# Performance work log

Hardware: AMD Instinct MI355X
Metric: run time of the kernel (lower is better)

Reference implementation:

```python
import jax, jax.numpy as jnp
import numpy as np

B, T, C, HR = 8, 4096, 256, 4
N_LAYER, LAYER_ID = 12, 3
HID = HR * C


def _fancy_decay_first():
    # Faithful reproduction of VRWKV_SpatialMix._init_weights(init_mode='fancy')
    r01 = LAYER_ID / (N_LAYER - 1)
    h = np.arange(C, dtype=np.float32)
    decay = -5.0 + 8.0 * (h / (C - 1)) ** (0.7 + 1.3 * r01)
    zig = ((np.arange(1, C + 1) % 3) - 1).astype(np.float32) * 0.5
    first = np.float32(np.log(0.3)) + zig
    return jnp.asarray(decay, jnp.float32), jnp.asarray(first, jnp.float32)


def setup_inputs() -> dict:
    key = jax.random.key(0)
    ks = jax.random.split(key, 12)
    s = 0.02  # small weight scale keeps exp(k) well-conditioned
    decay, first = _fancy_decay_first()
    return {
        "x": jax.random.normal(ks[0], (B, T, C), jnp.float32),
        "Wk": jax.random.normal(ks[1], (C, C), jnp.float32) * s,
        "Wv": jax.random.normal(ks[2], (C, C), jnp.float32) * s,
        "Wr": jax.random.normal(ks[3], (C, C), jnp.float32) * s,
        "Wo": jax.random.normal(ks[4], (C, C), jnp.float32) * s,
        "Wk_ffn": jax.random.normal(ks[5], (C, HID), jnp.float32) * s,
        "Wv_ffn": jax.random.normal(ks[6], (HID, C), jnp.float32) * s,
        "Wr_ffn": jax.random.normal(ks[7], (C, C), jnp.float32) * s,
        "g1": 1.0 + 0.1 * jax.random.normal(ks[8], (C,), jnp.float32),
        "b1": 0.1 * jax.random.normal(ks[9], (C,), jnp.float32),
        "g2": 1.0 + 0.1 * jax.random.normal(ks[10], (C,), jnp.float32),
        "b2": 0.1 * jax.random.normal(ks[11], (C,), jnp.float32),
        "spatial_decay": decay,
        "spatial_first": first,
    }


def _ln(x, g, b):
    m = jnp.mean(x, axis=-1, keepdims=True)
    v = jnp.var(x, axis=-1, keepdims=True)
    return (x - m) * jax.lax.rsqrt(v + 1e-5) * g + b


def _wkv(w, u, k, v):
    # Numerically-stable log-space WKV recurrence (same math as wkv_cuda):
    # y_t = (sum_{i<t} e^{w*(t-1-i)+k_i} v_i + e^{u+k_t} v_t)
    #     / (sum_{i<t} e^{w*(t-1-i)+k_i}     + e^{u+k_t})
    # w,u: [C]; k,v: [B,T,C] -> y: [B,T,C]
    Bb, Tt, Cc = k.shape
    kT = jnp.swapaxes(k, 0, 1)  # [T,B,C]
    vT = jnp.swapaxes(v, 0, 1)

    def step(carry, kv):
        p, q, o = carry           # [B,C] num / den / running max exponent
        kt, vt = kv               # [B,C]
        no = jnp.maximum(o, u + kt)
        A = jnp.exp(o - no)
        E = jnp.exp(u + kt - no)
        y = (A * p + E * vt) / (A * q + E)
        no2 = jnp.maximum(w + o, kt)
        A2 = jnp.exp(w + o - no2)
        E2 = jnp.exp(kt - no2)
        return (A2 * p + E2 * vt, A2 * q + E2, no2), y

    init = (jnp.zeros((Bb, Cc), k.dtype),
            jnp.zeros((Bb, Cc), k.dtype),
            jnp.full((Bb, Cc), -1e38, k.dtype))
    _, yT = jax.lax.scan(step, init, (kT, vT))
    return jnp.swapaxes(yT, 0, 1)


def reference(x, Wk, Wv, Wr, Wo, Wk_ffn, Wv_ffn, Wr_ffn, g1, b1, g2, b2,
              spatial_decay, spatial_first):
    Tlen = x.shape[1]
    # --- SpatialMix (shift_pixel=0 -> xk=xv=xr=h, key_norm=False) ---
    h = _ln(x, g1, b1)
    k = h @ Wk
    v = h @ Wv
    sr = jax.nn.sigmoid(h @ Wr)
    y = _wkv(spatial_decay / Tlen, spatial_first / Tlen, k, v)
    x = x + (sr * y) @ Wo
    # --- ChannelMix (square-ReLU MLP, sigmoid receptance gate) ---
    h2 = _ln(x, g2, b2)
    kk = jnp.square(jax.nn.relu(h2 @ Wk_ffn))
    x = x + jax.nn.sigmoid(h2 @ Wr_ffn) * (kk @ Wv_ffn)
    return x
```

## Files before the change

### kernel.cpp

```cpp
#include <hip/hip_runtime.h>
#include <hip/hip_bf16.h>
#include <math.h>

#define TDIM 4096
#define CDIM 256
#define BDIM 8
#define NTOK (BDIM * TDIM)
#define HIDDIM 1024
#define NCHUNK 256
#define CHLEN 16

typedef float f32x4 __attribute__((ext_vector_type(4)));
typedef __bf16 bf16x8 __attribute__((ext_vector_type(8)));
typedef __bf16 bf16x4 __attribute__((ext_vector_type(4)));

#define GLDS16(gp, lp) __builtin_amdgcn_global_load_lds( \
    (const __attribute__((address_space(1))) void*)(gp), \
    (__attribute__((address_space(3))) void*)(lp), 16, 0, 0)

#define WAITCNT_VM6  0x0F76
#define WAITCNT_VM5  0x0F75
#define WAITCNT_VM4  0x0F74
#define WAITCNT_VM2  0x0F72
#define WAITCNT_VM0  0x0F70
#define WAITCNT_VM20 0x4F74

__device__ __forceinline__ float sigm(float v) { return 1.0f / (1.0f + __expf(-v)); }

__global__ __launch_bounds__(256) void pack_weights(
    const float* __restrict__ Wk, const float* __restrict__ Wv,
    const float* __restrict__ Wr, const float* __restrict__ Wo,
    const float* __restrict__ Wkf, const float* __restrict__ Wvf,
    const float* __restrict__ Wrf,
    __bf16* __restrict__ WkvrT, __bf16* __restrict__ WoT,
    __bf16* __restrict__ Wkfr, unsigned char* __restrict__ Wvf8) {
  long long j = (long long)blockIdx.x * 256 + threadIdx.x;
  if (j < 196608) {
    int n = (int)(j >> 8), k = (int)(j & 255);
    const float* src = (n < 256) ? Wk : (n < 512 ? Wv : Wr);
    WkvrT[j] = (__bf16)src[k * 256 + (n & 255)];
    return;
  }
  j -= 196608;
  if (j < 65536) { int n = (int)(j >> 8), k = (int)(j & 255);
    WoT[j] = (__bf16)Wo[k * 256 + n]; return; }
  j -= 65536;
  if (j < 327680) { int n = (int)(j >> 8), k = (int)(j & 255);
    Wkfr[j] = (__bf16)(n < 1024 ? Wkf[(long long)k * 1024 + n]
                                : Wrf[k * 256 + (n - 1024)]);
    return; }
  j -= 327680;
  if (j < 65536) {
    const long long d = j * 4;
    const int n = (int)(d >> 10), k0 = (int)(d & 1023);
    int w = 0;
    w = __builtin_amdgcn_cvt_pk_fp8_f32(Wvf[(long long)k0 * 256 + n],
                                        Wvf[(long long)(k0 + 1) * 256 + n], w, false);
    w = __builtin_amdgcn_cvt_pk_fp8_f32(Wvf[(long long)(k0 + 2) * 256 + n],
                                        Wvf[(long long)(k0 + 3) * 256 + n], w, true);
    *(int*)&Wvf8[d] = w;
    return;
  }
}

__global__ __launch_bounds__(256) void ln_kernel(
    const float* __restrict__ x, const float* __restrict__ gamma,
    const float* __restrict__ beta, __bf16* __restrict__ h) {
  const int wave = threadIdx.x >> 6, lane = threadIdx.x & 63;
  const long long row = (long long)blockIdx.x * 4 + wave;
  const long long base = row * CDIM + lane * 4;
  const f32x4 v = *(const f32x4*)&x[base];
  float s = v[0] + v[1] + v[2] + v[3];
  float s2 = v[0]*v[0] + v[1]*v[1] + v[2]*v[2] + v[3]*v[3];
  #pragma unroll
  for (int o = 1; o < 64; o <<= 1) { s += __shfl_xor(s, o); s2 += __shfl_xor(s2, o); }
  const float mean = s * (1.0f / CDIM);
  const float var = s2 * (1.0f / CDIM) - mean * mean;
  const float rstd = rsqrtf(var + 1e-5f);
  const f32x4 g4 = *(const f32x4*)&gamma[lane * 4];
  const f32x4 b4 = *(const f32x4*)&beta[lane * 4];
  bf16x4 o;
  #pragma unroll
  for (int r = 0; r < 4; r++) o[r] = (__bf16)((v[r] - mean) * rstd * g4[r] + b4[r]);
  *(bf16x4*)&h[base] = o;
}

template <int BN, int EPI, int MT>
__global__ __launch_bounds__(256, 3) void gemm3(
    const __bf16* __restrict__ A, const __bf16* __restrict__ Bt,
    int M, int N,
    __bf16* __restrict__ outH, __bf16* __restrict__ outH2,
    unsigned char* __restrict__ outC) {
  constexpr int K = 256;
  constexpr int WNT = BN / 32;
  constexpr int NBC = BN / 64;
  __shared__ __bf16 sA[3][128 * 32];
  __shared__ __bf16 sB[3][BN * 32];

  const int tid = threadIdx.x;
  const int wave = tid >> 6, lane = tid & 63;
  const int quad = lane >> 4, mrow = lane & 15;
  const long long bm = (long long)blockIdx.x * (128 * MT);
  const long long bn = (long long)blockIdx.y * BN;
  const int wm = (wave & 1) * 64, wn = (wave >> 1) * (BN / 2);

  const int lrow = lane >> 2;
  const int lk = (lane & 3) * 8;

  auto issue = [&](int g) {
    const int buf = g % 3;
    const long long k0 = (long long)(g & 7) * 32;
    const long long ar = bm + (long long)(g >> 3) * 128;
    const int a0 = wave * 32;
    GLDS16(A + (ar + a0 + lrow) * (long long)K + k0 + lk, &sA[buf][a0 * 32]);
    GLDS16(A + (ar + a0 + 16 + lrow) * (long long)K + k0 + lk, &sA[buf][(a0 + 16) * 32]);
    #pragma unroll
    for (int bc = 0; bc < NBC; bc++) {
      const int r0 = wave * (BN / 4) + bc * 16;
      GLDS16(Bt + (bn + r0 + lrow) * (long long)K + k0 + lk, &sB[buf][r0 * 32]);
    }
  };

  f32x4 acc[4][WNT] = {};

  auto compute = [&](int g) {
    const int buf = g % 3;
    bf16x8 fa[4], fb[WNT];
    #pragma unroll
    for (int mt = 0; mt < 4; mt++)
      fa[mt] = *(const bf16x8*)&sA[buf][(wm + mt * 16 + mrow) * 32 + quad * 8];
    #pragma unroll
    for (int nt = 0; nt < WNT; nt++)
      fb[nt] = *(const bf16x8*)&sB[buf][(wn + nt * 16 + mrow) * 32 + quad * 8];
    #pragma unroll
    for (int mt = 0; mt < 4; mt++)
      #pragma unroll
      for (int nt = 0; nt < WNT; nt++)
        acc[mt][nt] = __builtin_amdgcn_mfma_f32_16x16x32_bf16(fb[nt], fa[mt], acc[mt][nt], 0, 0, 0);
  };

  auto epilogue = [&](int mti) {
    const long long rb0 = bm + (long long)mti * 128;
    #pragma unroll
    for (int mt = 0; mt < 4; mt++) {
      #pragma unroll
      for (int nt = 0; nt < WNT; nt++) {
        const long long row = rb0 + wm + mt * 16 + mrow;
        const int cloc = wn + nt * 16 + quad * 4;
        const long long colb = bn + cloc;
        const f32x4 a = acc[mt][nt];
        if (EPI == 0) {
          const int plane = blockIdx.y >> 1;
          __bf16* o = outH + (long long)plane * ((long long)M * 256);
          const long long c2 = colb & 255;
          bf16x4 v;
          if (plane == 2) {
            #pragma unroll
            for (int r = 0; r < 4; r++) v[r] = (__bf16)sigm(a[r]);
          } else {
            #pragma unroll
            for (int r = 0; r < 4; r++) v[r] = (__bf16)a[r];
          }
          *(bf16x4*)&o[row * 256 + c2] = v;
        } else if (EPI == 2) {
          if (blockIdx.y < 8) {
            float t0 = a[0] > 0.0f ? a[0] : 0.0f;
            float t1 = a[1] > 0.0f ? a[1] : 0.0f;
            float t2 = a[2] > 0.0f ? a[2] : 0.0f;
            float t3 = a[3] > 0.0f ? a[3] : 0.0f;
            int w = 0;
            w = __builtin_amdgcn_cvt_pk_fp8_f32(t0 * t0, t1 * t1, w, false);
            w = __builtin_amdgcn_cvt_pk_fp8_f32(t2 * t2, t3 * t3, w, true);
            *(int*)&outC[row * 1024 + colb] = w;
          } else {
            bf16x4 v;
            #pragma unroll
            for (int r = 0; r < 4; r++) v[r] = (__bf16)sigm(a[r]);
            *(bf16x4*)&outH2[row * 256 + (colb - 1024)] = v;
          }
        }
        acc[mt][nt] = (f32x4){0.0f, 0.0f, 0.0f, 0.0f};
      }
    }
  };

  constexpr int total = 8 * MT;
  issue(0);
  issue(1);

  #pragma unroll 1
  for (int g = 0; g < total; g++) {
    if (g == total - 1) {
      __builtin_amdgcn_s_waitcnt(WAITCNT_VM0);
    } else if (MT > 1 && g >= 8 && (g & 7) <= 1) {
      __builtin_amdgcn_s_waitcnt(WAITCNT_VM20);
    } else if (BN == 256) {
      __builtin_amdgcn_s_waitcnt(WAITCNT_VM6);
    } else {
      __builtin_amdgcn_s_waitcnt(WAITCNT_VM4);
    }
    __builtin_amdgcn_s_barrier();
    if (g + 2 < total) issue(g + 2);
    compute(g);
    if ((g & 7) == 7) epilogue(g >> 3);
  }
}

__global__ __launch_bounds__(256, 2) void gemm7(
    const __bf16* __restrict__ A, const __bf16* __restrict__ Bt,
    const float* __restrict__ x,
    const float* __restrict__ gammaP, const float* __restrict__ betaP,
    __bf16* __restrict__ x1h, __bf16* __restrict__ h2) {
  constexpr int K = 256;
  __shared__ __bf16 sA[3][64 * 32];
  __shared__ __bf16 sB[3][256 * 32];
  __shared__ float redS[4][64], redQ[4][64];

  const int tid = threadIdx.x;
  const int wave = tid >> 6, lane = tid & 63;
  const int quad = lane >> 4, mrow = lane & 15;
  const long long bm = (long long)blockIdx.x * 64;
  const int wn = wave * 64;
  const int lrow = lane >> 2;
  const int lk = (lane & 3) * 8;

  auto issue = [&](int g) {
    const int buf = g % 3;
    const long long k0 = (long long)g * 32;
    GLDS16(A + (bm + wave * 16 + lrow) * (long long)K + k0 + lk,
           &sA[buf][(wave * 16) * 32]);
    #pragma unroll
    for (int bc = 0; bc < 4; bc++) {
      const int r0 = wave * 64 + bc * 16;
      GLDS16(Bt + (r0 + lrow) * (long long)K + k0 + lk, &sB[buf][r0 * 32]);
    }
  };

  f32x4 acc[4][4] = {};

  auto compute = [&](int g) {
    const int buf = g % 3;
    bf16x8 fa[4], fb[4];
    #pragma unroll
    for (int mt = 0; mt < 4; mt++)
      fa[mt] = *(const bf16x8*)&sA[buf][(mt * 16 + mrow) * 32 + quad * 8];
    #pragma unroll
    for (int nt = 0; nt < 4; nt++)
      fb[nt] = *(const bf16x8*)&sB[buf][(wn + nt * 16 + mrow) * 32 + quad * 8];
    #pragma unroll
    for (int mt = 0; mt < 4; mt++)
      #pragma unroll
      for (int nt = 0; nt < 4; nt++)
        acc[mt][nt] = __builtin_amdgcn_mfma_f32_16x16x32_bf16(fb[nt], fa[mt], acc[mt][nt], 0, 0, 0);
  };

  issue(0);
  issue(1);
  #pragma unroll 1
  for (int g = 0; g < 8; g++) {
    if (g == 7) {
      __builtin_amdgcn_s_waitcnt(WAITCNT_VM0);
    } else {
      __builtin_amdgcn_s_waitcnt(WAITCNT_VM5);
    }
    __builtin_amdgcn_s_barrier();
    if (g + 2 < 8) issue(g + 2);
    compute(g);
  }

  float sum[4] = {0, 0, 0, 0}, sq[4] = {0, 0, 0, 0};
  #pragma unroll
  for (int mt = 0; mt < 4; mt++) {
    #pragma unroll
    for (int nt = 0; nt < 4; nt++) {
      const long long row = bm + mt * 16 + mrow;
      const long long colb = wn + nt * 16 + quad * 4;
      acc[mt][nt] += *(const f32x4*)&x[row * 256 + colb];
      #pragma unroll
      for (int r = 0; r < 4; r++) {
        sum[mt] += acc[mt][nt][r];
        sq[mt] += acc[mt][nt][r] * acc[mt][nt][r];
      }
    }
  }
  #pragma unroll
  for (int mt = 0; mt < 4; mt++) {
    sum[mt] += __shfl_xor(sum[mt], 16); sq[mt] += __shfl_xor(sq[mt], 16);
    sum[mt] += __shfl_xor(sum[mt], 32); sq[mt] += __shfl_xor(sq[mt], 32);
  }
  if (quad == 0) {
    #pragma unroll
    for (int mt = 0; mt < 4; mt++) {
      redS[wave][mt * 16 + mrow] = sum[mt];
      redQ[wave][mt * 16 + mrow] = sq[mt];
    }
  }
  __syncthreads();
  #pragma unroll
  for (int mt = 0; mt < 4; mt++) {
    const int rb = mt * 16 + mrow;
    const float ts = redS[0][rb] + redS[1][rb] + redS[2][rb] + redS[3][rb];
    const float tq = redQ[0][rb] + redQ[1][rb] + redQ[2][rb] + redQ[3][rb];
    const float mean = ts * (1.0f / 256.0f);
    const float rstd = rsqrtf(tq * (1.0f / 256.0f) - mean * mean + 1e-5f);
    const long long row = bm + rb;
    #pragma unroll
    for (int nt = 0; nt < 4; nt++) {
      const long long colb = wn + nt * 16 + quad * 4;
      const f32x4 g4 = *(const f32x4*)&gammaP[colb];
      const f32x4 b4 = *(const f32x4*)&betaP[colb];
      bf16x4 xo, ho;
      #pragma unroll
      for (int r = 0; r < 4; r++) {
        const float t = acc[mt][nt][r];
        xo[r] = (__bf16)t;
        ho[r] = (__bf16)((t - mean) * rstd * g4[r] + b4[r]);
      }
      *(bf16x4*)&x1h[row * 256 + colb] = xo;
      *(bf16x4*)&h2[row * 256 + colb] = ho;
    }
  }
}

__global__ __launch_bounds__(256, 4) void gemm6(
    const unsigned char* __restrict__ A8, const unsigned char* __restrict__ B8,
    float* __restrict__ outF, const __bf16* __restrict__ srcH,
    const __bf16* __restrict__ gate) {
  __shared__ unsigned char sA[3][128 * 32];
  __shared__ unsigned char sB[3][128 * 32];
  const int tid = threadIdx.x;
  const int wave = tid >> 6, lane = tid & 63;
  const int quad = lane >> 4, mrow = lane & 15;
  const long long bm = (long long)blockIdx.x * 128;
  const long long bn = (long long)blockIdx.y * 128;
  const int wm = (wave & 1) * 64, wn = (wave >> 1) * 64;
  const int srow = lane >> 1;
  const int hs = (lane & 1) ^ ((lane >> 2) & 1);

  auto issue = [&](int g) {
    const int buf = g % 3;
    const long long k0 = (long long)g * 32;
    const int a0 = wave * 32;
    GLDS16(A8 + (bm + a0 + srow) * 1024LL + k0 + hs * 16, &sA[buf][a0 * 32]);
    GLDS16(B8 + (bn + a0 + srow) * 1024LL + k0 + hs * 16, &sB[buf][a0 * 32]);
  };

  f32x4 acc[4][4] = {};
  issue(0);
  issue(1);
  const int sw = (mrow >> 1) & 1;

  auto compute = [&](int i) {
    const int buf = i % 3;
    long long fa[4], fb[4];
    const int off = ((((quad >> 1) ^ sw) << 4) | ((quad & 1) << 3));
    #pragma unroll
    for (int mt = 0; mt < 4; mt++)
      fa[mt] = *(const long long*)&sA[buf][(wm + mt * 16 + mrow) * 32 + off];
    #pragma unroll
    for (int nt = 0; nt < 4; nt++)
      fb[nt] = *(const long long*)&sB[buf][(wn + nt * 16 + mrow) * 32 + off];
    #pragma unroll
    for (int mt = 0; mt < 4; mt++)
      #pragma unroll
      for (int nt = 0; nt < 4; nt++)
        acc[mt][nt] = __builtin_amdgcn_mfma_f32_16x16x32_fp8_fp8(fb[nt], fa[mt], acc[mt][nt], 0, 0, 0);
  };

  #pragma unroll 1
  for (int i = 0; i < 31; i++) {
    __builtin_amdgcn_s_waitcnt(WAITCNT_VM2);
    __builtin_amdgcn_s_barrier();
    if (i + 2 < 32) issue(i + 2);
    compute(i);
  }
  __builtin_amdgcn_s_waitcnt(WAITCNT_VM0);
  __builtin_amdgcn_s_barrier();
  compute(31);

  #pragma unroll
  for (int mt = 0; mt < 4; mt++) {
    #pragma unroll
    for (int nt = 0; nt < 4; nt++) {
      const long long row = bm + wm + mt * 16 + mrow;
      const long long colb = bn + wn + nt * 16 + quad * 4;
      const long long idx = row * 256 + colb;
      const f32x4 a = acc[mt][nt];
      const bf16x4 s4 = *(const bf16x4*)&srcH[idx];
      const bf16x4 g4 = *(const bf16x4*)&gate[idx];
      f32x4 v;
      #pragma unroll
      for (int r = 0; r < 4; r++) v[r] = (float)s4[r] + (float)g4[r] * a[r];
      *(f32x4*)&outF[idx] = v;
    }
  }
}

__global__ __launch_bounds__(256) void wkv_phase1(
    const __bf16* __restrict__ ka, const __bf16* __restrict__ va,
    const float* __restrict__ decay,
    float* __restrict__ Sloc, float* __restrict__ Zloc) {
  const int wave = threadIdx.x >> 6, lane = threadIdx.x & 63;
  const int gi = blockIdx.x * 4 + wave;
  const int b = gi >> 8, chunk = gi & (NCHUNK - 1);
  const int c0 = lane * 4;
  const f32x4 w4 = *(const f32x4*)&decay[c0];
  f32x4 ew;
  #pragma unroll
  for (int r = 0; r < 4; r++) ew[r] = __expf(w4[r] * (1.0f / TDIM));
  f32x4 S = {0,0,0,0}, Z = {0,0,0,0};
  long long base = ((long long)b * TDIM + (long long)chunk * CHLEN) * 256 + c0;
  #pragma unroll 4
  for (int t = 0; t < CHLEN; t++) {
    const bf16x4 k4 = *(const bf16x4*)&ka[base + (long long)t * 256];
    const bf16x4 v4 = *(const bf16x4*)&va[base + (long long)t * 256];
    #pragma unroll
    for (int r = 0; r < 4; r++) {
      const float ek = __expf((float)k4[r]);
      S[r] = ew[r] * S[r] + ek * (float)v4[r];
      Z[r] = ew[r] * Z[r] + ek;
    }
  }
  const long long o = (long long)gi * 256 + c0;
  *(f32x4*)&Sloc[o] = S;
  *(f32x4*)&Zloc[o] = Z;
}

__global__ __launch_bounds__(256) void wkv_phase2(
    const float* __restrict__ Sloc, const float* __restrict__ Zloc,
    const float* __restrict__ decay,
    float* __restrict__ Sstart, float* __restrict__ Zstart) {
  const int idx = blockIdx.x * 256 + threadIdx.x;
  const int c = idx & 255;
  const int b = idx >> 8;
  const float w = decay[c] * (1.0f / TDIM);
  const float ewL = __expf(w * (float)CHLEN);
  float S = 0.0f, Z = 0.0f;
  for (int j = 0; j < NCHUNK; j++) {
    const long long o = ((long long)b * NCHUNK + j) * 256 + c;
    Sstart[o] = S;
    Zstart[o] = Z;
    S = ewL * S + Sloc[o];
    Z = ewL * Z + Zloc[o];
  }
}

__global__ __launch_bounds__(256) void wkv_phase3(
    const __bf16* __restrict__ ka, const __bf16* __restrict__ va,
    const __bf16* __restrict__ ra,
    const float* __restrict__ decay, const float* __restrict__ first,
    const float* __restrict__ Sstart, const float* __restrict__ Zstart,
    __bf16* __restrict__ a2) {
  const int wave = threadIdx.x >> 6, lane = threadIdx.x & 63;
  const int gi = blockIdx.x * 4 + wave;
  const int b = gi >> 8, chunk = gi & (NCHUNK - 1);
  const int c0 = lane * 4;
  const f32x4 w4 = *(const f32x4*)&decay[c0];
  const f32x4 u4 = *(const f32x4*)&first[c0];
  f32x4 ew, eu;
  #pragma unroll
  for (int r = 0; r < 4; r++) {
    ew[r] = __expf(w4[r] * (1.0f / TDIM));
    eu[r] = __expf(u4[r] * (1.0f / TDIM));
  }
  const long long so = (long long)gi * 256 + c0;
  f32x4 S = *(const f32x4*)&Sstart[so];
  f32x4 Z = *(const f32x4*)&Zstart[so];
  long long base = ((long long)b * TDIM + (long long)chunk * CHLEN) * 256 + c0;
  #pragma unroll 2
  for (int t = 0; t < CHLEN; t++) {
    const long long p = base + (long long)t * 256;
    const bf16x4 k4 = *(const bf16x4*)&ka[p];
    const bf16x4 v4 = *(const bf16x4*)&va[p];
    const bf16x4 r4 = *(const bf16x4*)&ra[p];
    bf16x4 o;
    #pragma unroll
    for (int r = 0; r < 4; r++) {
      const float ek = __expf((float)k4[r]);
      const float E = eu[r] * ek;
      const float y = (S[r] + E * (float)v4[r]) / (Z[r] + E);
      o[r] = (__bf16)((float)r4[r] * y);
      S[r] = ew[r] * S[r] + ek * (float)v4[r];
      Z[r] = ew[r] * Z[r] + ek;
    }
    *(bf16x4*)&a2[p] = o;
  }
}

extern "C" void kernel_launch(void* const* d_in, const int* in_sizes, int n_in,
                              void* d_out, int out_size, void* d_ws, size_t ws_size,
                              hipStream_t stream) {
  const float* x     = (const float*)d_in[0];
  const float* Wk    = (const float*)d_in[1];
  const float* Wv    = (const float*)d_in[2];
  const float* Wr    = (const float*)d_in[3];
  const float* Wo    = (const float*)d_in[4];
  const float* Wkf   = (const float*)d_in[5];
  const float* Wvf   = (const float*)d_in[6];
  const float* Wrf   = (const float*)d_in[7];
  const float* g1    = (const float*)d_in[8];
  const float* b1    = (const float*)d_in[9];
  const float* g2    = (const float*)d_in[10];
  const float* b2    = (const float*)d_in[11];
  const float* decay = (const float*)d_in[12];
  const float* first = (const float*)d_in[13];
  float* out = (float*)d_out;
  char* ws = (char*)d_ws;

  __bf16* ka     = (__bf16*)(ws + 0);
  __bf16* va     = (__bf16*)(ws + 16777216LL);
  __bf16* ra     = (__bf16*)(ws + 33554432LL);
  __bf16* a2     = (__bf16*)(ws + 50331648LL);
  __bf16* g2buf  = (__bf16*)(ws + 50331648LL);
  __bf16* hbuf   = (__bf16*)(ws + 67108864LL);
  __bf16* h2     = (__bf16*)(ws + 67108864LL);
  __bf16* x1h    = (__bf16*)(ws + 83886080LL);
  unsigned char* kk8 = (unsigned char*)(ws + 100663296LL);
  float*  Sloc   = (float*)(ws + 134217728LL);
  float*  Zloc   = (float*)(ws + 137363456LL);
  float*  Sstart = (float*)(ws + 140509184LL);
  float*  Zstart = (float*)(ws + 143654912LL);
  __bf16* WkvrT  = (__bf16*)(ws + 167772160LL);
  __bf16* WoT    = (__bf16*)(ws + 168165376LL);
  __bf16* Wkfr   = (__bf16*)(ws + 168296448LL);
  unsigned char* Wvf8 = (unsigned char*)(ws + 168951808LL);

  pack_weights<<<2560, 256, 0, stream>>>(Wk, Wv, Wr, Wo, Wkf, Wvf, Wrf,
                                         WkvrT, WoT, Wkfr, Wvf8);

  ln_kernel<<<NTOK / 4, 256, 0, stream>>>(x, g1, b1, hbuf);
  gemm3<128, 0, 2><<<dim3(NTOK / 256, 6), 256, 0, stream>>>(
      hbuf, WkvrT, NTOK, 768, ka, nullptr, nullptr);
  wkv_phase1<<<BDIM * NCHUNK / 4, 256, 0, stream>>>(ka, va, decay, Sloc, Zloc);
  wkv_phase2<<<BDIM, 256, 0, stream>>>(Sloc, Zloc, decay, Sstart, Zstart);
  wkv_phase3<<<BDIM * NCHUNK / 4, 256, 0, stream>>>(ka, va, ra, decay, first,
                                                    Sstart, Zstart, a2);
  gemm7<<<NTOK / 64, 256, 0, stream>>>(a2, WoT, x, g2, b2, x1h, h2);

  gemm3<128, 2, 2><<<dim3(NTOK / 256, 10), 256, 0, stream>>>(
      h2, Wkfr, NTOK, 1280, nullptr, g2buf, kk8);
  gemm6<<<dim3(NTOK / 128, 2), 256, 0, stream>>>(
      kk8, Wvf8, out, x1h, g2buf);
}
```

Before: 279.1 us.

## Switch LN outputs and K/V/R and FFN-in GEMMs to FP8 MFMA

Both layer-norm outputs (LN1 and the LN2 fused into gemm7) are now written as FP8, and the K/V/R and FFN key/receptance weights are packed to FP8. The bf16 gemm3 kernel is replaced by an FP8 gemm8 with 128x128 tiles and swizzled LDS reads, modeled on the existing gemm6. This halves activation and weight traffic and uses the higher-rate FP8 MFMA, at the cost of lower precision on the k, v and r projections that feed the exponential WKV recurrence.

Result: faster. 270.3 us (-3.1%).

```diff
diff --git a/kernel.cpp b/kernel.cpp
--- a/kernel.cpp
+++ b/kernel.cpp
@@ -18,12 +18,9 @@
     (const __attribute__((address_space(1))) void*)(gp), \
     (__attribute__((address_space(3))) void*)(lp), 16, 0, 0)
 
-#define WAITCNT_VM6  0x0F76
 #define WAITCNT_VM5  0x0F75
-#define WAITCNT_VM4  0x0F74
 #define WAITCNT_VM2  0x0F72
 #define WAITCNT_VM0  0x0F70
-#define WAITCNT_VM20 0x4F74
 
 __device__ __forceinline__ float sigm(float v) { return 1.0f / (1.0f + __expf(-v)); }
 
@@ -32,24 +29,45 @@
     const float* __restrict__ Wr, const float* __restrict__ Wo,
     const float* __restrict__ Wkf, const float* __restrict__ Wvf,
     const float* __restrict__ Wrf,
-    __bf16* __restrict__ WkvrT, __bf16* __restrict__ WoT,
-    __bf16* __restrict__ Wkfr, unsigned char* __restrict__ Wvf8) {
+    __bf16* __restrict__ WoT, unsigned char* __restrict__ Wkvr8,
+    unsigned char* __restrict__ Wkfr8, unsigned char* __restrict__ Wvf8) {
   long long j = (long long)blockIdx.x * 256 + threadIdx.x;
-  if (j < 196608) {
-    int n = (int)(j >> 8), k = (int)(j & 255);
+  if (j < 49152) {
+    const long long d = j * 4;
+    const int n = (int)(d >> 8), k0 = (int)(d & 255);
     const float* src = (n < 256) ? Wk : (n < 512 ? Wv : Wr);
-    WkvrT[j] = (__bf16)src[k * 256 + (n & 255)];
+    const int nn = n & 255;
+    int w = 0;
+    w = __builtin_amdgcn_cvt_pk_fp8_f32(src[k0 * 256 + nn],
+                                        src[(k0 + 1) * 256 + nn], w, false);
+    w = __builtin_amdgcn_cvt_pk_fp8_f32(src[(k0 + 2) * 256 + nn],
+                                        src[(k0 + 3) * 256 + nn], w, true);
+    *(int*)&Wkvr8[d] = w;
     return;
   }
-  j -= 196608;
+  j -= 49152;
   if (j < 65536) { int n = (int)(j >> 8), k = (int)(j & 255);
     WoT[j] = (__bf16)Wo[k * 256 + n]; return; }
   j -= 65536;
-  if (j < 327680) { int n = (int)(j >> 8), k = (int)(j & 255);
-    Wkfr[j] = (__bf16)(n < 1024 ? Wkf[(long long)k * 1024 + n]
-                                : Wrf[k * 256 + (n - 1024)]);
-    return; }
-  j -= 327680;
+  if (j < 81920) {
+    const long long d = j * 4;
+    const int n = (int)(d >> 8), k0 = (int)(d & 255);
+    float v0, v1, v2, v3;
+    if (n < 1024) {
+      v0 = Wkf[(long long)k0 * 1024 + n];       v1 = Wkf[(long long)(k0 + 1) * 1024 + n];
+      v2 = Wkf[(long long)(k0 + 2) * 1024 + n]; v3 = Wkf[(long long)(k0 + 3) * 1024 + n];
+    } else {
+      const int m = n - 1024;
+      v0 = Wrf[k0 * 256 + m];       v1 = Wrf[(k0 + 1) * 256 + m];
+      v2 = Wrf[(k0 + 2) * 256 + m]; v3 = Wrf[(k0 + 3) * 256 + m];
+    }
+    int w = 0;
+    w = __builtin_amdgcn_cvt_pk_fp8_f32(v0, v1, w, false);
+    w = __builtin_amdgcn_cvt_pk_fp8_f32(v2, v3, w, true);
+    *(int*)&Wkfr8[d] = w;
+    return;
+  }
+  j -= 81920;
   if (j < 65536) {
     const long long d = j * 4;
     const int n = (int)(d >> 10), k0 = (int)(d & 1023);
@@ -65,7 +83,7 @@
 
 __global__ __launch_bounds__(256) void ln_kernel(
     const float* __restrict__ x, const float* __restrict__ gamma,
-    const float* __restrict__ beta, __bf16* __restrict__ h) {
+    const float* __restrict__ beta, unsigned char* __restrict__ h8) {
   const int wave = threadIdx.x >> 6, lane = threadIdx.x & 63;
   const long long row = (long long)blockIdx.x * 4 + wave;
   const long long base = row * CDIM + lane * 4;
@@ -79,130 +97,111 @@
   const float rstd = rsqrtf(var + 1e-5f);
   const f32x4 g4 = *(const f32x4*)&gamma[lane * 4];
   const f32x4 b4 = *(const f32x4*)&beta[lane * 4];
-  bf16x4 o;
-  #pragma unroll
-  for (int r = 0; r < 4; r++) o[r] = (__bf16)((v[r] - mean) * rstd * g4[r] + b4[r]);
-  *(bf16x4*)&h[base] = o;
-}
-
-template <int BN, int EPI, int MT>
-__global__ __launch_bounds__(256, 3) void gemm3(
-    const __bf16* __restrict__ A, const __bf16* __restrict__ Bt,
-    int M, int N,
-    __bf16* __restrict__ outH, __bf16* __restrict__ outH2,
+  float o0 = (v[0] - mean) * rstd * g4[0] + b4[0];
+  float o1 = (v[1] - mean) * rstd * g4[1] + b4[1];
+  float o2 = (v[2] - mean) * rstd * g4[2] + b4[2];
+  float o3 = (v[3] - mean) * rstd * g4[3] + b4[3];
+  int w = 0;
+  w = __builtin_amdgcn_cvt_pk_fp8_f32(o0, o1, w, false);
+  w = __builtin_amdgcn_cvt_pk_fp8_f32(o2, o3, w, true);
+  *(int*)&h8[base] = w;
+}
+
+template <int EPI>
+__global__ __launch_bounds__(256, 4) void gemm8(
+    const unsigned char* __restrict__ A8, const unsigned char* __restrict__ B8,
+    int M, __bf16* __restrict__ outH, __bf16* __restrict__ outH2,
     unsigned char* __restrict__ outC) {
-  constexpr int K = 256;
-  constexpr int WNT = BN / 32;
-  constexpr int NBC = BN / 64;
-  __shared__ __bf16 sA[3][128 * 32];
-  __shared__ __bf16 sB[3][BN * 32];
-
+  __shared__ unsigned char sA[3][128 * 32];
+  __shared__ unsigned char sB[3][128 * 32];
   const int tid = threadIdx.x;
   const int wave = tid >> 6, lane = tid & 63;
   const int quad = lane >> 4, mrow = lane & 15;
-  const long long bm = (long long)blockIdx.x * (128 * MT);
-  const long long bn = (long long)blockIdx.y * BN;
-  const int wm = (wave & 1) * 64, wn = (wave >> 1) * (BN / 2);
-
-  const int lrow = lane >> 2;
-  const int lk = (lane & 3) * 8;
+  const long long bm = (long long)blockIdx.x * 128;
+  const long long bn = (long long)blockIdx.y * 128;
+  const int wm = (wave & 1) * 64, wn = (wave >> 1) * 64;
+  const int srow = lane >> 1;
+  const int hs = (lane & 1) ^ ((lane >> 2) & 1);
 
   auto issue = [&](int g) {
     const int buf = g % 3;
-    const long long k0 = (long long)(g & 7) * 32;
-    const long long ar = bm + (long long)(g >> 3) * 128;
+    const long long k0 = (long long)g * 32;
     const int a0 = wave * 32;
-    GLDS16(A + (ar + a0 + lrow) * (long long)K + k0 + lk, &sA[buf][a0 * 32]);
-    GLDS16(A + (ar + a0 + 16 + lrow) * (long long)K + k0 + lk, &sA[buf][(a0 + 16) * 32]);
-    #pragma unroll
-    for (int bc = 0; bc < NBC; bc++) {
-      const int r0 = wave * (BN / 4) + bc * 16;
-      GLDS16(Bt + (bn + r0 + lrow) * (long long)K + k0 + lk, &sB[buf][r0 * 32]);
-    }
+    GLDS16(A8 + (bm + a0 + srow) * 256LL + k0 + hs * 16, &sA[buf][a0 * 32]);
+    GLDS16(B8 + (bn + a0 + srow) * 256LL + k0 + hs * 16, &sB[buf][a0 * 32]);
   };
 
-  f32x4 acc[4][WNT] = {};
-
-  auto compute = [&](int g) {
-    const int buf = g % 3;
-    bf16x8 fa[4], fb[WNT];
+  f32x4 acc[4][4] = {};
+  issue(0);
+  issue(1);
+  const int sw = (mrow >> 1) & 1;
+
+  auto compute = [&](int i) {
+    const int buf = i % 3;
+    long long fa[4], fb[4];
+    const int off = ((((quad >> 1) ^ sw) << 4) | ((quad & 1) << 3));
     #pragma unroll
     for (int mt = 0; mt < 4; mt++)
-      fa[mt] = *(const bf16x8*)&sA[buf][(wm + mt * 16 + mrow) * 32 + quad * 8];
-    #pragma unroll
-    for (int nt = 0; nt < WNT; nt++)
-      fb[nt] = *(const bf16x8*)&sB[buf][(wn + nt * 16 + mrow) * 32 + quad * 8];
+      fa[mt] = *(const long long*)&sA[buf][(wm + mt * 16 + mrow) * 32 + off];
+    #pragma unroll
+    for (int nt = 0; nt < 4; nt++)
+      fb[nt] = *(const long long*)&sB[buf][(wn + nt * 16 + mrow) * 32 + off];
     #pragma unroll
     for (int mt = 0; mt < 4; mt++)
       #pragma unroll
-      for (int nt = 0; nt < WNT; nt++)
-        acc[mt][nt] = __builtin_amdgcn_mfma_f32_16x16x32_bf16(fb[nt], fa[mt], acc[mt][nt], 0, 0, 0);
+      for (int nt = 0; nt < 4; nt++)
+        acc[mt][nt] = __builtin_amdgcn_mfma_f32_16x16x32_fp8_fp8(fb[nt], fa[mt], acc[mt][nt], 0, 0, 0);
   };
 
-  auto epilogue = [&](int mti) {
-    const long long rb0 = bm + (long long)mti * 128;
-    #pragma unroll
-    for (int mt = 0; mt < 4; mt++) {
-      #pragma unroll
-      for (int nt = 0; nt < WNT; nt++) {
-        const long long row = rb0 + wm + mt * 16 + mrow;
-        const int cloc = wn + nt * 16 + quad * 4;
-        const long long colb = bn + cloc;
-        const f32x4 a = acc[mt][nt];
-        if (EPI == 0) {
-          const int plane = blockIdx.y >> 1;
-          __bf16* o = outH + (long long)plane * ((long long)M * 256);
-          const long long c2 = colb & 255;
+  #pragma unroll 1
+  for (int i = 0; i < 7; i++) {
+    __builtin_amdgcn_s_waitcnt(WAITCNT_VM2);
+    __builtin_amdgcn_s_barrier();
+    if (i + 2 < 8) issue(i + 2);
+    compute(i);
+  }
+  __builtin_amdgcn_s_waitcnt(WAITCNT_VM0);
+  __builtin_amdgcn_s_barrier();
+  compute(7);
+
+  #pragma unroll
+  for (int mt = 0; mt < 4; mt++) {
+    #pragma unroll
+    for (int nt = 0; nt < 4; nt++) {
+      const long long row = bm + wm + mt * 16 + mrow;
+      const long long colb = bn + wn + nt * 16 + quad * 4;
+      const f32x4 a = acc[mt][nt];
+      if (EPI == 0) {
+        const int plane = blockIdx.y >> 1;
+        __bf16* o = outH + (long long)plane * ((long long)M * 256);
+        const long long c2 = colb & 255;
+        bf16x4 v;
+        if (plane == 2) {
+          #pragma unroll
+          for (int r = 0; r < 4; r++) v[r] = (__bf16)sigm(a[r]);
+        } else {
+          #pragma unroll
+          for (int r = 0; r < 4; r++) v[r] = (__bf16)a[r];
+        }
+        *(bf16x4*)&o[row * 256 + c2] = v;
+      } else {
+        if (blockIdx.y < 8) {
+          float t0 = a[0] > 0.0f ? a[0] : 0.0f;
+          float t1 = a[1] > 0.0f ? a[1] : 0.0f;
+          float t2 = a[2] > 0.0f ? a[2] : 0.0f;
+          float t3 = a[3] > 0.0f ? a[3] : 0.0f;
+          int w = 0;
+          w = __builtin_amdgcn_cvt_pk_fp8_f32(t0 * t0, t1 * t1, w, false);
+          w = __builtin_amdgcn_cvt_pk_fp8_f32(t2 * t2, t3 * t3, w, true);
+          *(int*)&outC[row * 1024 + colb] = w;
+        } else {
           bf16x4 v;
-          if (plane == 2) {
-            #pragma unroll
-            for (int r = 0; r < 4; r++) v[r] = (__bf16)sigm(a[r]);
-          } else {
-            #pragma unroll
-            for (int r = 0; r < 4; r++) v[r] = (__bf16)a[r];
-          }
-          *(bf16x4*)&o[row * 256 + c2] = v;
-        } else if (EPI == 2) {
-          if (blockIdx.y < 8) {
-            float t0 = a[0] > 0.0f ? a[0] : 0.0f;
-            float t1 = a[1] > 0.0f ? a[1] : 0.0f;
-            float t2 = a[2] > 0.0f ? a[2] : 0.0f;
-            float t3 = a[3] > 0.0f ? a[3] : 0.0f;
-            int w = 0;
-            w = __builtin_amdgcn_cvt_pk_fp8_f32(t0 * t0, t1 * t1, w, false);
-            w = __builtin_amdgcn_cvt_pk_fp8_f32(t2 * t2, t3 * t3, w, true);
-            *(int*)&outC[row * 1024 + colb] = w;
-          } else {
-            bf16x4 v;
-            #pragma unroll
-            for (int r = 0; r < 4; r++) v[r] = (__bf16)sigm(a[r]);
-            *(bf16x4*)&outH2[row * 256 + (colb - 1024)] = v;
-          }
+          #pragma unroll
+          for (int r = 0; r < 4; r++) v[r] = (__bf16)sigm(a[r]);
+          *(bf16x4*)&outH2[row * 256 + (colb - 1024)] = v;
         }
-        acc[mt][nt] = (f32x4){0.0f, 0.0f, 0.0f, 0.0f};
       }
     }
-  };
-
-  constexpr int total = 8 * MT;
-  issue(0);
-  issue(1);
-
-  #pragma unroll 1
-  for (int g = 0; g < total; g++) {
-    if (g == total - 1) {
-      __builtin_amdgcn_s_waitcnt(WAITCNT_VM0);
-    } else if (MT > 1 && g >= 8 && (g & 7) <= 1) {
-      __builtin_amdgcn_s_waitcnt(WAITCNT_VM20);
-    } else if (BN == 256) {
-      __builtin_amdgcn_s_waitcnt(WAITCNT_VM6);
-    } else {
-      __builtin_amdgcn_s_waitcnt(WAITCNT_VM4);
-    }
-    __builtin_amdgcn_s_barrier();
-    if (g + 2 < total) issue(g + 2);
-    compute(g);
-    if ((g & 7) == 7) epilogue(g >> 3);
   }
 }
 
@@ -210,7 +209,7 @@
     const __bf16* __restrict__ A, const __bf16* __restrict__ Bt,
     const float* __restrict__ x,
     const float* __restrict__ gammaP, const float* __restrict__ betaP,
-    __bf16* __restrict__ x1h, __bf16* __restrict__ h2) {
+    __bf16* __restrict__ x1h, unsigned char* __restrict__ h28) {
   constexpr int K = 256;
   __shared__ __bf16 sA[3][64 * 32];
   __shared__ __bf16 sB[3][256 * 32];
@@ -309,15 +308,22 @@
       const long long colb = wn + nt * 16 + quad * 4;
       const f32x4 g4 = *(const f32x4*)&gammaP[colb];
       const f32x4 b4 = *(const f32x4*)&betaP[colb];
-      bf16x4 xo, ho;
-      #pragma unroll
-      for (int r = 0; r < 4; r++) {
-        const float t = acc[mt][nt][r];
-        xo[r] = (__bf16)t;
-        ho[r] = (__bf16)((t - mean) * rstd * g4[r] + b4[r]);
+      bf16x4 xo;
+      float h0, h1, h2v, h3;
+      {
+        const float t0 = acc[mt][nt][0], t1 = acc[mt][nt][1];
+        const float t2 = acc[mt][nt][2], t3 = acc[mt][nt][3];
+        xo[0] = (__bf16)t0; xo[1] = (__bf16)t1; xo[2] = (__bf16)t2; xo[3] = (__bf16)t3;
+        h0 = (t0 - mean) * rstd * g4[0] + b4[0];
+        h1 = (t1 - mean) * rstd * g4[1] + b4[1];
+        h2v = (t2 - mean) * rstd * g4[2] + b4[2];
+        h3 = (t3 - mean) * rstd * g4[3] + b4[3];
       }
       *(bf16x4*)&x1h[row * 256 + colb] = xo;
-      *(bf16x4*)&h2[row * 256 + colb] = ho;
+      int w = 0;
+      w = __builtin_amdgcn_cvt_pk_fp8_f32(h0, h1, w, false);
+      w = __builtin_amdgcn_cvt_pk_fp8_f32(h2v, h3, w, true);
+      *(int*)&h28[row * 256 + colb] = w;
     }
   }
 }
@@ -512,33 +518,33 @@
   __bf16* ra     = (__bf16*)(ws + 33554432LL);
   __bf16* a2     = (__bf16*)(ws + 50331648LL);
   __bf16* g2buf  = (__bf16*)(ws + 50331648LL);
-  __bf16* hbuf   = (__bf16*)(ws + 67108864LL);
-  __bf16* h2     = (__bf16*)(ws + 67108864LL);
+  unsigned char* h8  = (unsigned char*)(ws + 67108864LL);
+  unsigned char* h28 = (unsigned char*)(ws + 67108864LL);
   __bf16* x1h    = (__bf16*)(ws + 83886080LL);
   unsigned char* kk8 = (unsigned char*)(ws + 100663296LL);
   float*  Sloc   = (float*)(ws + 134217728LL);
   float*  Zloc   = (float*)(ws + 137363456LL);
   float*  Sstart = (float*)(ws + 140509184LL);
   float*  Zstart = (float*)(ws + 143654912LL);
-  __bf16* WkvrT  = (__bf16*)(ws + 167772160LL);
-  __bf16* WoT    = (__bf16*)(ws + 168165376LL);
-  __bf16* Wkfr   = (__bf16*)(ws + 168296448LL);
-  unsigned char* Wvf8 = (unsigned char*)(ws + 168951808LL);
-
-  pack_weights<<<2560, 256, 0, stream>>>(Wk, Wv, Wr, Wo, Wkf, Wvf, Wrf,
-                                         WkvrT, WoT, Wkfr, Wvf8);
-
-  ln_kernel<<<NTOK / 4, 256, 0, stream>>>(x, g1, b1, hbuf);
-  gemm3<128, 0, 2><<<dim3(NTOK / 256, 6), 256, 0, stream>>>(
-      hbuf, WkvrT, NTOK, 768, ka, nullptr, nullptr);
+  __bf16* WoT    = (__bf16*)(ws + 167772160LL);
+  unsigned char* Wkvr8 = (unsigned char*)(ws + 167903232LL);
+  unsigned char* Wkfr8 = (unsigned char*)(ws + 168099840LL);
+  unsigned char* Wvf8  = (unsigned char*)(ws + 168427520LL);
+
+  pack_weights<<<1024, 256, 0, stream>>>(Wk, Wv, Wr, Wo, Wkf, Wvf, Wrf,
+                                         WoT, Wkvr8, Wkfr8, Wvf8);
+
+  ln_kernel<<<NTOK / 4, 256, 0, stream>>>(x, g1, b1, h8);
+  gemm8<0><<<dim3(NTOK / 128, 6), 256, 0, stream>>>(
+      h8, Wkvr8, NTOK, ka, nullptr, nullptr);
   wkv_phase1<<<BDIM * NCHUNK / 4, 256, 0, stream>>>(ka, va, decay, Sloc, Zloc);
   wkv_phase2<<<BDIM, 256, 0, stream>>>(Sloc, Zloc, decay, Sstart, Zstart);
   wkv_phase3<<<BDIM * NCHUNK / 4, 256, 0, stream>>>(ka, va, ra, decay, first,
                                                     Sstart, Zstart, a2);
-  gemm7<<<NTOK / 64, 256, 0, stream>>>(a2, WoT, x, g2, b2, x1h, h2);
-
-  gemm3<128, 2, 2><<<dim3(NTOK / 256, 10), 256, 0, stream>>>(
-      h2, Wkfr, NTOK, 1280, nullptr, g2buf, kk8);
+  gemm7<<<NTOK / 64, 256, 0, stream>>>(a2, WoT, x, g2, b2, x1h, h28);
+
+  gemm8<2><<<dim3(NTOK / 128, 10), 256, 0, stream>>>(
+      h28, Wkfr8, NTOK, nullptr, g2buf, kk8);
   gemm6<<<dim3(NTOK / 128, 2), 256, 0, stream>>>(
       kk8, Wvf8, out, x1h, g2buf);
 }
```
